# Optimization experiments

Measured on AMD Instinct MI355X. Metric: run time of the kernel, lower is better.

Reference implementation:

```python
import jax, jax.numpy as jnp
import numpy as np

IOU_THRESHOLD = 0.5
BOX_W, OBJ_W, CLS_W = 3.54, 64.3, 37.4
B, N, NS, NA, NC = 16, 32, 3, 3, 80
IMG = 512.0

ANCHORS_PX = np.array([[[10, 13], [16, 30], [33, 23]],
                       [[30, 61], [62, 45], [59, 119]],
                       [[116, 90], [156, 198], [373, 326]]], dtype=np.float32)
STRIDES = np.array([8.0, 16.0, 32.0], dtype=np.float32)


def setup_inputs() -> dict:
    key = jax.random.key(0)
    ks = jax.random.split(key, 6)
    infs = {}
    for s, g in enumerate([64, 32, 16]):
        infs[f"inf{s}"] = jax.random.normal(ks[s], (B, NA, g, g, 5 + NC), dtype=jnp.float32)
    xy = jax.random.uniform(ks[3], (B, N, 2), minval=0.0, maxval=IMG)
    wh = jax.random.uniform(ks[4], (B, N, 2), minval=8.0, maxval=96.0)
    cls_id = jax.random.randint(ks[5], (B, N, 1), 0, NC).astype(jnp.float32)
    targets = jnp.concatenate([xy, wh, cls_id], axis=-1)  # [B,N,5] xywh(px)+class
    return {"inf0": infs["inf0"], "inf1": infs["inf1"], "inf2": infs["inf2"],
            "anchors": jnp.asarray(ANCHORS_PX), "strides": jnp.asarray(STRIDES),
            "targets": targets}


def xywh2rect(b):
    xy, wh = b[..., 0:2], b[..., 2:4]
    return jnp.concatenate([xy - wh / 2, xy + wh / 2], axis=-1)


def jaccard(a1, a2):
    x0 = jnp.maximum(a1[..., 0], a2[..., 0]); y0 = jnp.maximum(a1[..., 1], a2[..., 1])
    x1 = jnp.minimum(a1[..., 2], a2[..., 2]); y1 = jnp.minimum(a1[..., 3], a2[..., 3])
    inter = (x1 - x0) * (y1 - y0) * ((x0 < x1) & (y0 < y1)).astype(a1.dtype)
    area = lambda r: (r[..., 2] - r[..., 0]) * (r[..., 3] - r[..., 1])
    union = area(a1) + area(a2) - inter
    return inter / union


def bce_logits(p, t):
    # pos_weight == 1.0 for both obj and cls heads
    return t * jax.nn.softplus(-p) + (1.0 - t) * jax.nn.softplus(p)


def reference(inf0, inf1, inf2, anchors, strides, targets):
    inference = [inf0, inf1, inf2]
    nb, nt, _ = targets.shape
    ns, na, _ = anchors.shape
    nc = inf0.shape[-1] - 5
    # compress targets: all targets assumed valid (no -1 padding)
    bidx = jnp.repeat(jnp.arange(nb), nt)            # [n]
    flat = targets.reshape(-1, 5)                     # [n,5]
    cls_id = flat[:, 4].astype(jnp.int32)             # [n]
    boxes = flat[:, 0:4]                              # [n,4] xywh px
    # per-scale target boxes in grid units, xy -> cell offset
    tb = boxes[:, None, :] / strides[None, :, None]   # [n,ns,4]
    c = jnp.floor(tb[..., 0:2])
    tb = jnp.concatenate([tb[..., 0:2] - c, tb[..., 2:4]], axis=-1)
    ci = c[..., 0].astype(jnp.int32)                  # [n,ns]
    cj = c[..., 1].astype(jnp.int32)
    # anchors in grid units with center 0.5
    anc = jnp.concatenate([jnp.full((ns, na, 2), 0.5, anchors.dtype),
                           anchors / strides[:, None, None]], axis=-1)
    # anchor matching: [n,ns,na]
    obj = jaccard(xywh2rect(tb)[:, :, None, :], xywh2rect(anc)[None]) > IOU_THRESHOLD
    a_idx = jnp.arange(na)
    box_loss = 0.0; obj_loss = 0.0; cls_loss = 0.0
    for s in range(ns):
        inf = inference[s]                            # [B,na,H,W,5+nc]
        mf = obj[:, s, :].astype(jnp.float32)         # [n,na]
        cnt = jnp.maximum(mf.sum(), 1.0)
        b, cis, cjs = bidx, ci[:, s], cj[:, s]
        pred = inf[b[:, None], a_idx[None, :], cjs[:, None], cis[:, None]]  # [n,na,5+nc]
        # decode box
        p_xy = jax.nn.sigmoid(pred[..., 0:2])
        p_wh = jnp.minimum(jnp.exp(pred[..., 2:4]), 1000.0) * anc[s, :, 2:4][None]
        p_box = jnp.concatenate([p_xy, p_wh], axis=-1)        # [n,na,4]
        t_box = jnp.broadcast_to(tb[:, s, None, :], p_box.shape)
        iou = jaccard(xywh2rect(p_box), xywh2rect(t_box))      # [n,na]
        box_loss = box_loss + jnp.sum((1.0 - iou) * mf) / cnt
        # objectness target: scatter 1 at matched cells
        t_obj = jnp.zeros(inf.shape[:-1], jnp.float32)
        t_obj = t_obj.at[b[:, None], a_idx[None, :], cjs[:, None], cis[:, None]].max(mf)
        obj_loss = obj_loss + jnp.mean(bce_logits(inf[..., 4], t_obj))
        # class loss over matched rows only
        t_cls = jnp.broadcast_to(jax.nn.one_hot(cls_id, nc)[:, None, :], pred[..., 5:].shape)
        cls_bce = bce_logits(pred[..., 5:], t_cls)             # [n,na,nc]
        cls_loss = cls_loss + jnp.sum(cls_bce * mf[..., None]) / (cnt * nc)
    return box_loss * BOX_W + obj_loss * OBJ_W + cls_loss * CLS_W
```

## Files before the change

### kernel.cpp

```cpp
#include <hip/hip_runtime.h>

constexpr int S0 = 16 * 3 * 64 * 64;
constexpr int S1 = 16 * 3 * 32 * 32;
constexpr int S2 = 16 * 3 * 16 * 16;
constexpr int TOT = S0 + S1 + S2;

constexpr int DBLOCKS = TOT / 1024;
constexpr int DB0 = S0 / 1024;
constexpr int DB1 = DB0 + S1 / 1024;

constexpr int TWAVES  = 512 * 9;
constexpr int TBLOCKS = TWAVES / 4;

constexpr int WS_OBJ = TBLOCKS * 10;

__device__ __forceinline__ float softplusf(float x) {
    return fmaxf(x, 0.0f) + __logf(1.0f + __expf(-fabsf(x)));
}

__device__ __forceinline__ bool anchor_hit(
    float x, float y, float w, float h, float st, float aw, float ah,
    int& ci, int& cj, float& fx, float& fy, float& tbw, float& tbh)
{
    const float tbx = x / st, tby = y / st;
    tbw = w / st; tbh = h / st;
    const float cif = floorf(tbx), cjf = floorf(tby);
    ci = (int)cif; cj = (int)cjf;
    fx = tbx - cif; fy = tby - cjf;
    const float tx0 = fx - tbw*0.5f, ty0 = fy - tbh*0.5f;
    const float tx1 = fx + tbw*0.5f, ty1 = fy + tbh*0.5f;
    const float ax0 = 0.5f - aw*0.5f, ay0 = 0.5f - ah*0.5f;
    const float ax1 = 0.5f + aw*0.5f, ay1 = 0.5f + ah*0.5f;
    const float ix0 = fmaxf(tx0, ax0), iy0 = fmaxf(ty0, ay0);
    const float ix1 = fminf(tx1, ax1), iy1 = fminf(ty1, ay1);
    float inter = (ix1-ix0)*(iy1-iy0);
    inter = (ix0 < ix1 && iy0 < iy1) ? inter : 0.0f;
    const float iou = inter / (tbw*tbh + aw*ah - inter);
    return iou > 0.5f;
}

__global__ __launch_bounds__(256) void yolo_main_kernel(
    const float* __restrict__ inf0, const float* __restrict__ inf1,
    const float* __restrict__ inf2, const float* __restrict__ anchors,
    const float* __restrict__ strides, const float* __restrict__ targets,
    float* __restrict__ ws)
{
    if (blockIdx.x < DBLOCKS) {
        const int bi = blockIdx.x;
        const float* inf; int base; float w;
        if (bi < DB0)      { inf = inf0; base = bi * 1024;          w = 1.0f/(float)S0; }
        else if (bi < DB1) { inf = inf1; base = (bi - DB0) * 1024;  w = 1.0f/(float)S1; }
        else               { inf = inf2; base = (bi - DB1) * 1024;  w = 1.0f/(float)S2; }
        const int l0 = base + threadIdx.x;
        const float a0 = inf[(long)(l0      ) * 85 + 4];
        const float a1 = inf[(long)(l0 + 256) * 85 + 4];
        const float a2 = inf[(long)(l0 + 512) * 85 + 4];
        const float a3 = inf[(long)(l0 + 768) * 85 + 4];
        float v = softplusf(a0) + softplusf(a1) + softplusf(a2) + softplusf(a3);
        #pragma unroll
        for (int off = 32; off > 0; off >>= 1) v += __shfl_down(v, off, 64);
        __shared__ float wsum[4];
        const int lane = threadIdx.x & 63, wid = threadIdx.x >> 6;
        if (lane == 0) wsum[wid] = v;
        __syncthreads();
        if (threadIdx.x == 0)
            ws[WS_OBJ + bi] = (wsum[0] + wsum[1] + wsum[2] + wsum[3]) * w;
    } else {
        __shared__ float s_part[10];
        if (threadIdx.x < 10) s_part[threadIdx.x] = 0.0f;
        __syncthreads();

        const int tb   = blockIdx.x - DBLOCKS;
        const int wave = tb * 4 + (threadIdx.x >> 6);
        const int lane = threadIdx.x & 63;
        const int t  = wave / 9;
        const int sa = wave - 9 * t;
        const int s  = sa / 3;
        const int a  = sa - 3 * s;
        const int b  = t >> 5;

        const float x = targets[t*5+0];
        const float y = targets[t*5+1];
        const float w = targets[t*5+2];
        const float h = targets[t*5+3];
        const int cls = (int)targets[t*5+4];

        const float st = strides[s];
        const float aw = anchors[(s*3+a)*2+0] / st;
        const float ah = anchors[(s*3+a)*2+1] / st;

        int ci, cj; float fx, fy, tbw, tbh;
        const bool hit = anchor_hit(x, y, w, h, st, aw, ah,
                                    ci, cj, fx, fy, tbw, tbh);
        if (hit) {
            const int g = (s == 0) ? 64 : (s == 1) ? 32 : 16;
            const float* inf = (s == 0) ? inf0 : (s == 1) ? inf1 : inf2;
            const float invM = (s == 0) ? 1.0f/(float)S0
                             : (s == 1) ? 1.0f/(float)S1 : 1.0f/(float)S2;

            const int cellflat = ((b*3 + a)*g + cj)*g + ci;
            const float* pred = inf + (long)cellflat * 85;

            const float p4 = pred[4];
            const float px = 1.0f / (1.0f + __expf(-pred[0]));
            const float py = 1.0f / (1.0f + __expf(-pred[1]));
            const float pw = fminf(__expf(pred[2]), 1000.0f) * aw;
            const float ph = fminf(__expf(pred[3]), 1000.0f) * ah;
            const float tx0 = fx - tbw*0.5f, ty0 = fy - tbh*0.5f;
            const float tx1 = fx + tbw*0.5f, ty1 = fy + tbh*0.5f;
            const float bx0 = px - pw*0.5f, by0 = py - ph*0.5f;
            const float bx1 = px + pw*0.5f, by1 = py + ph*0.5f;
            const float jx0 = fmaxf(bx0, tx0), jy0 = fmaxf(by0, ty0);
            const float jx1 = fminf(bx1, tx1), jy1 = fminf(by1, ty1);
            float inter2 = (jx1-jx0)*(jy1-jy0);
            inter2 = (jx0 < jx1 && jy0 < jy1) ? inter2 : 0.0f;
            const float iou2 = inter2 / (pw*ph + tbw*tbh - inter2);

            float v = softplusf(pred[5 + lane]);
            if (lane == cls) v -= pred[5 + cls];
            if (lane < 16) {
                const int c2 = 64 + lane;
                v += softplusf(pred[5 + c2]);
                if (c2 == cls) v -= pred[5 + c2];
            }
            #pragma unroll
            for (int off = 32; off > 0; off >>= 1) v += __shfl_down(v, off, 64);

            bool dup = false;
            if (lane < (t & 31)) {
                const int t2 = (b << 5) + lane;
                const float x2 = targets[t2*5+0];
                const float y2 = targets[t2*5+1];
                const float w2 = targets[t2*5+2];
                const float h2 = targets[t2*5+3];
                int ci2, cj2; float fx2, fy2, tbw2, tbh2;
                const bool hit2 = anchor_hit(x2, y2, w2, h2, st, aw, ah,
                                             ci2, cj2, fx2, fy2, tbw2, tbh2);
                dup = hit2 && (ci2 == ci) && (cj2 == cj);
            }
            const unsigned long long m = __ballot(dup);

            if (lane == 0) {
                atomicAdd(&s_part[1 + s], 1.0f);
                atomicAdd(&s_part[4 + s], 1.0f - iou2);
                atomicAdd(&s_part[7 + s], v);
                if (m == 0ull) atomicAdd(&s_part[0], -p4 * invM);
            }
        }
        __syncthreads();
        if (threadIdx.x < 10)
            ws[tb * 10 + threadIdx.x] = s_part[threadIdx.x];
    }
}

__global__ __launch_bounds__(256) void yolo_finalize_kernel(
    const float* __restrict__ ws, float* __restrict__ out)
{
    float acc[10];
    #pragma unroll
    for (int c = 0; c < 10; ++c) acc[c] = 0.0f;
    for (int r = threadIdx.x; r < TBLOCKS; r += 256) {
        #pragma unroll
        for (int c = 0; c < 10; ++c) acc[c] += ws[r * 10 + c];
    }
    float obj = 0.0f;
    for (int i = threadIdx.x; i < DBLOCKS; i += 256) obj += ws[WS_OBJ + i];
    acc[0] += obj;

    #pragma unroll
    for (int c = 0; c < 10; ++c) {
        float v = acc[c];
        #pragma unroll
        for (int off = 32; off > 0; off >>= 1) v += __shfl_down(v, off, 64);
        acc[c] = v;
    }
    __shared__ float red[4][10];
    const int lane = threadIdx.x & 63, wid = threadIdx.x >> 6;
    if (lane == 0) {
        #pragma unroll
        for (int c = 0; c < 10; ++c) red[wid][c] = acc[c];
    }
    __syncthreads();
    if (threadIdx.x == 0) {
        float tt[10];
        #pragma unroll
        for (int c = 0; c < 10; ++c)
            tt[c] = red[0][c] + red[1][c] + red[2][c] + red[3][c];
        float box = 0.0f, cls = 0.0f;
        #pragma unroll
        for (int s = 0; s < 3; ++s) {
            const float cnt = fmaxf(tt[1 + s], 1.0f);
            box += tt[4 + s] / cnt;
            cls += tt[7 + s] / (cnt * 80.0f);
        }
        out[0] = 3.54f * box + 64.3f * tt[0] + 37.4f * cls;
    }
}

extern "C" void kernel_launch(void* const* d_in, const int* in_sizes, int n_in,
                              void* d_out, int out_size, void* d_ws, size_t ws_size,
                              hipStream_t stream) {
    const float* inf0    = (const float*)d_in[0];
    const float* inf1    = (const float*)d_in[1];
    const float* inf2    = (const float*)d_in[2];
    const float* anchors = (const float*)d_in[3];
    const float* strides = (const float*)d_in[4];
    const float* targets = (const float*)d_in[5];
    float* ws  = (float*)d_ws;
    float* out = (float*)d_out;

    yolo_main_kernel<<<DBLOCKS + TBLOCKS, 256, 0, stream>>>(
        inf0, inf1, inf2, anchors, strides, targets, ws);
    yolo_finalize_kernel<<<1, 256, 0, stream>>>(ws, out);
}
```

Baseline: 113.4 us.

## Process all nine scale-anchor pairs per wave and double obj elements per block

New measurement: 112.5 us, median of 2. About the same (-0.8%).

```diff
diff --git a/kernel.cpp b/kernel.cpp
--- a/kernel.cpp
+++ b/kernel.cpp
@@ -5,12 +5,11 @@
 constexpr int S2 = 16 * 3 * 16 * 16;
 constexpr int TOT = S0 + S1 + S2;
 
-constexpr int DBLOCKS = TOT / 1024;
-constexpr int DB0 = S0 / 1024;
-constexpr int DB1 = DB0 + S1 / 1024;
-
-constexpr int TWAVES  = 512 * 9;
-constexpr int TBLOCKS = TWAVES / 4;
+constexpr int DBLOCKS = TOT / 2048;
+constexpr int DB0 = S0 / 2048;
+constexpr int DB1 = DB0 + S1 / 2048;
+
+constexpr int TBLOCKS = 512 / 4;
 
 constexpr int WS_OBJ = TBLOCKS * 10;
 
@@ -48,15 +47,14 @@
     if (blockIdx.x < DBLOCKS) {
         const int bi = blockIdx.x;
         const float* inf; int base; float w;
-        if (bi < DB0)      { inf = inf0; base = bi * 1024;          w = 1.0f/(float)S0; }
-        else if (bi < DB1) { inf = inf1; base = (bi - DB0) * 1024;  w = 1.0f/(float)S1; }
-        else               { inf = inf2; base = (bi - DB1) * 1024;  w = 1.0f/(float)S2; }
+        if (bi < DB0)      { inf = inf0; base = bi * 2048;          w = 1.0f/(float)S0; }
+        else if (bi < DB1) { inf = inf1; base = (bi - DB0) * 2048;  w = 1.0f/(float)S1; }
+        else               { inf = inf2; base = (bi - DB1) * 2048;  w = 1.0f/(float)S2; }
         const int l0 = base + threadIdx.x;
-        const float a0 = inf[(long)(l0      ) * 85 + 4];
-        const float a1 = inf[(long)(l0 + 256) * 85 + 4];
-        const float a2 = inf[(long)(l0 + 512) * 85 + 4];
-        const float a3 = inf[(long)(l0 + 768) * 85 + 4];
-        float v = softplusf(a0) + softplusf(a1) + softplusf(a2) + softplusf(a3);
+        float v = 0.0f;
+        #pragma unroll
+        for (int k = 0; k < 8; ++k)
+            v += softplusf(inf[(long)(l0 + k * 256) * 85 + 4]);
         #pragma unroll
         for (int off = 32; off > 0; off >>= 1) v += __shfl_down(v, off, 64);
         __shared__ float wsum[4];
@@ -66,18 +64,11 @@
         if (threadIdx.x == 0)
             ws[WS_OBJ + bi] = (wsum[0] + wsum[1] + wsum[2] + wsum[3]) * w;
     } else {
-        __shared__ float s_part[10];
-        if (threadIdx.x < 10) s_part[threadIdx.x] = 0.0f;
-        __syncthreads();
-
         const int tb   = blockIdx.x - DBLOCKS;
-        const int wave = tb * 4 + (threadIdx.x >> 6);
+        const int wid  = threadIdx.x >> 6;
         const int lane = threadIdx.x & 63;
-        const int t  = wave / 9;
-        const int sa = wave - 9 * t;
-        const int s  = sa / 3;
-        const int a  = sa - 3 * s;
-        const int b  = t >> 5;
+        const int t    = tb * 4 + wid;
+        const int b    = t >> 5;
 
         const float x = targets[t*5+0];
         const float y = targets[t*5+1];
@@ -85,71 +76,87 @@
         const float h = targets[t*5+3];
         const int cls = (int)targets[t*5+4];
 
-        const float st = strides[s];
-        const float aw = anchors[(s*3+a)*2+0] / st;
-        const float ah = anchors[(s*3+a)*2+1] / st;
-
-        int ci, cj; float fx, fy, tbw, tbh;
-        const bool hit = anchor_hit(x, y, w, h, st, aw, ah,
-                                    ci, cj, fx, fy, tbw, tbh);
-        if (hit) {
-            const int g = (s == 0) ? 64 : (s == 1) ? 32 : 16;
-            const float* inf = (s == 0) ? inf0 : (s == 1) ? inf1 : inf2;
-            const float invM = (s == 0) ? 1.0f/(float)S0
-                             : (s == 1) ? 1.0f/(float)S1 : 1.0f/(float)S2;
-
-            const int cellflat = ((b*3 + a)*g + cj)*g + ci;
-            const float* pred = inf + (long)cellflat * 85;
-
-            const float p4 = pred[4];
-            const float px = 1.0f / (1.0f + __expf(-pred[0]));
-            const float py = 1.0f / (1.0f + __expf(-pred[1]));
-            const float pw = fminf(__expf(pred[2]), 1000.0f) * aw;
-            const float ph = fminf(__expf(pred[3]), 1000.0f) * ah;
-            const float tx0 = fx - tbw*0.5f, ty0 = fy - tbh*0.5f;
-            const float tx1 = fx + tbw*0.5f, ty1 = fy + tbh*0.5f;
-            const float bx0 = px - pw*0.5f, by0 = py - ph*0.5f;
-            const float bx1 = px + pw*0.5f, by1 = py + ph*0.5f;
-            const float jx0 = fmaxf(bx0, tx0), jy0 = fmaxf(by0, ty0);
-            const float jx1 = fminf(bx1, tx1), jy1 = fminf(by1, ty1);
-            float inter2 = (jx1-jx0)*(jy1-jy0);
-            inter2 = (jx0 < jx1 && jy0 < jy1) ? inter2 : 0.0f;
-            const float iou2 = inter2 / (pw*ph + tbw*tbh - inter2);
-
-            float v = softplusf(pred[5 + lane]);
-            if (lane == cls) v -= pred[5 + cls];
-            if (lane < 16) {
-                const int c2 = 64 + lane;
-                v += softplusf(pred[5 + c2]);
-                if (c2 == cls) v -= pred[5 + c2];
+        float acc[10];
+        #pragma unroll
+        for (int c = 0; c < 10; ++c) acc[c] = 0.0f;
+
+        #pragma unroll
+        for (int sa = 0; sa < 9; ++sa) {
+            const int s = sa / 3;
+            const int a = sa - 3 * s;
+            const float st = strides[s];
+            const float aw = anchors[(s*3+a)*2+0] / st;
+            const float ah = anchors[(s*3+a)*2+1] / st;
+
+            int ci, cj; float fx, fy, tbw, tbh;
+            const bool hit = anchor_hit(x, y, w, h, st, aw, ah,
+                                        ci, cj, fx, fy, tbw, tbh);
+            if (hit) {
+                const int g = (s == 0) ? 64 : (s == 1) ? 32 : 16;
+                const float* inf = (s == 0) ? inf0 : (s == 1) ? inf1 : inf2;
+                const float invM = (s == 0) ? 1.0f/(float)S0
+                                 : (s == 1) ? 1.0f/(float)S1 : 1.0f/(float)S2;
+
+                const int cellflat = ((b*3 + a)*g + cj)*g + ci;
+                const float* pred = inf + (long)cellflat * 85;
+
+                const float p4 = pred[4];
+                const float px = 1.0f / (1.0f + __expf(-pred[0]));
+                const float py = 1.0f / (1.0f + __expf(-pred[1]));
+                const float pw = fminf(__expf(pred[2]), 1000.0f) * aw;
+                const float ph = fminf(__expf(pred[3]), 1000.0f) * ah;
+                const float tx0 = fx - tbw*0.5f, ty0 = fy - tbh*0.5f;
+                const float tx1 = fx + tbw*0.5f, ty1 = fy + tbh*0.5f;
+                const float bx0 = px - pw*0.5f, by0 = py - ph*0.5f;
+                const float bx1 = px + pw*0.5f, by1 = py + ph*0.5f;
+                const float jx0 = fmaxf(bx0, tx0), jy0 = fmaxf(by0, ty0);
+                const float jx1 = fminf(bx1, tx1), jy1 = fminf(by1, ty1);
+                float inter2 = (jx1-jx0)*(jy1-jy0);
+                inter2 = (jx0 < jx1 && jy0 < jy1) ? inter2 : 0.0f;
+                const float iou2 = inter2 / (pw*ph + tbw*tbh - inter2);
+
+                float v = softplusf(pred[5 + lane]);
+                if (lane == cls) v -= pred[5 + cls];
+                if (lane < 16) {
+                    const int c2 = 64 + lane;
+                    v += softplusf(pred[5 + c2]);
+                    if (c2 == cls) v -= pred[5 + c2];
+                }
+                #pragma unroll
+                for (int off = 32; off > 0; off >>= 1)
+                    v += __shfl_down(v, off, 64);
+
+                bool dup = false;
+                if (lane < (t & 31)) {
+                    const int t2 = (b << 5) + lane;
+                    const float x2 = targets[t2*5+0];
+                    const float y2 = targets[t2*5+1];
+                    const float w2 = targets[t2*5+2];
+                    const float h2 = targets[t2*5+3];
+                    int ci2, cj2; float fx2, fy2, tbw2, tbh2;
+                    const bool hit2 = anchor_hit(x2, y2, w2, h2, st, aw, ah,
+                                                 ci2, cj2, fx2, fy2, tbw2, tbh2);
+                    dup = hit2 && (ci2 == ci) && (cj2 == cj);
+                }
+                const unsigned long long m = __ballot(dup);
+
+                acc[1 + s] += 1.0f;
+                acc[4 + s] += 1.0f - iou2;
+                acc[7 + s] += v;
+                if (m == 0ull) acc[0] += -p4 * invM;
             }
+        }
+
+        __shared__ float rows[4][10];
+        if (lane == 0) {
             #pragma unroll
-            for (int off = 32; off > 0; off >>= 1) v += __shfl_down(v, off, 64);
-
-            bool dup = false;
-            if (lane < (t & 31)) {
-                const int t2 = (b << 5) + lane;
-                const float x2 = targets[t2*5+0];
-                const float y2 = targets[t2*5+1];
-                const float w2 = targets[t2*5+2];
-                const float h2 = targets[t2*5+3];
-                int ci2, cj2; float fx2, fy2, tbw2, tbh2;
-                const bool hit2 = anchor_hit(x2, y2, w2, h2, st, aw, ah,
-                                             ci2, cj2, fx2, fy2, tbw2, tbh2);
-                dup = hit2 && (ci2 == ci) && (cj2 == cj);
-            }
-            const unsigned long long m = __ballot(dup);
-
-            if (lane == 0) {
-                atomicAdd(&s_part[1 + s], 1.0f);
-                atomicAdd(&s_part[4 + s], 1.0f - iou2);
-                atomicAdd(&s_part[7 + s], v);
-                if (m == 0ull) atomicAdd(&s_part[0], -p4 * invM);
-            }
+            for (int c = 0; c < 10; ++c) rows[wid][c] = acc[c];
         }
         __syncthreads();
         if (threadIdx.x < 10)
-            ws[tb * 10 + threadIdx.x] = s_part[threadIdx.x];
+            ws[tb * 10 + threadIdx.x] = rows[0][threadIdx.x] +
+                rows[1][threadIdx.x] + rows[2][threadIdx.x] +
+                rows[3][threadIdx.x];
     }
 }
 
```
